# Kernel tuning notes

Measured on AMD Instinct MI355X. Metric: run time of the kernel, lower is better.

The kernel has to match this reference:

```python
import jax, jax.numpy as jnp
import numpy as np

# Forest of B perfect binary trees, depth D levels, M = 2**D - 1 nodes/tree.
B, D, H, X, VOCAB, NCLS = 32, 12, 256, 256, 32000, 20
M = 2 ** D - 1          # 4095 nodes per tree
N = B * M               # 131040 total nodes


def setup_inputs() -> dict:
    key = jax.random.key(0)
    ks = jax.random.split(key, 9)
    x = jax.random.randint(ks[0], (N,), 0, VOCAB, dtype=jnp.int32)
    # leaves are the last level of each tree: in-tree index >= 2**(D-1)-1
    leaf = (jnp.arange(M) >= 2 ** (D - 1) - 1).astype(jnp.int32)
    x_mask = jnp.tile(leaf, B)  # [N] int32, 1 on leaves, 0 on internal nodes
    s = 0.02
    Emb = jax.random.normal(ks[1], (VOCAB, X), jnp.float32) * s
    W_iou = jax.random.normal(ks[2], (3 * H, X), jnp.float32) * s
    b_iou = jnp.zeros((3 * H,), jnp.float32)
    U_iou = jax.random.normal(ks[3], (3 * H, H), jnp.float32) * s
    U_f = jax.random.normal(ks[4], (H, H), jnp.float32) * s
    b_f = jnp.ones((H,), jnp.float32)  # forget-gate bias init
    W_out = jax.random.normal(ks[5], (NCLS, H), jnp.float32) * s
    b_out = jnp.zeros((NCLS,), jnp.float32)
    return {"x": x, "x_mask": x_mask, "Emb": Emb, "W_iou": W_iou,
            "b_iou": b_iou, "U_iou": U_iou, "U_f": U_f, "b_f": b_f,
            "W_out": W_out, "b_out": b_out}


def reference(x, x_mask, Emb, W_iou, b_iou, U_iou, U_f, b_f, W_out, b_out):
    # input_module: embedding applied to masked ids, result masked again
    x_emb = Emb[x * x_mask] * x_mask[:, None].astype(Emb.dtype)      # [N, X]
    xiou = (x_emb @ W_iou.T).reshape(B, M, 3 * H)                    # W_iou * x per node
    h_sum = jnp.zeros((B, M, H), Emb.dtype)    # sum of children h (childsum)
    fc_sum = jnp.zeros((B, M, H), Emb.dtype)   # sum_k f_k * c_k from children
    h_all = jnp.zeros((B, M, H), Emb.dtype)
    # topological propagation: leaves (deepest level) -> roots
    for l in range(D - 1, -1, -1):
        s_, e_ = 2 ** l - 1, 2 ** (l + 1) - 1  # static in-tree level slice
        iou = xiou[:, s_:e_] + h_sum[:, s_:e_] @ U_iou.T + b_iou
        i, o, u = jnp.split(iou, 3, axis=-1)
        c = jax.nn.sigmoid(i) * jnp.tanh(u) + fc_sum[:, s_:e_]
        h = jax.nn.sigmoid(o) * jnp.tanh(c)
        h_all = h_all.at[:, s_:e_].set(h)
        if l > 0:
            f = jax.nn.sigmoid(h @ U_f.T + b_f)          # per-child forget gate
            parents = (np.arange(s_, e_) - 1) // 2       # static parent indices
            h_sum = h_sum.at[:, parents].add(h)
            fc_sum = fc_sum.at[:, parents].add(f * c)
    # output_module applied to all node states
    return h_all.reshape(N, H) @ W_out.T + b_out                    # [N, NCLS]
```

## Files before the change

kernel.cpp:

```cpp
#include <hip/hip_runtime.h>

#define B_TREES 32
#define DEPTH   12
#define M_NODES 4095
#define N_NODES (B_TREES * M_NODES)
#define HDIM    256
#define VOCAB   32000
#define NCLS    20
#define LEAFROWS 65536
#define LDSH_S 20

typedef _Float16 f16;
typedef _Float16 f16x8 __attribute__((ext_vector_type(8)));
typedef _Float16 f16x4 __attribute__((ext_vector_type(4)));
typedef _Float16 f16x2 __attribute__((ext_vector_type(2)));
typedef float    f32x4 __attribute__((ext_vector_type(4)));

__device__ __forceinline__ float sigf(float x)      { return 1.0f / (1.0f + __expf(-x)); }
__device__ __forceinline__ float tanh_fast(float x) { return 1.0f - 2.0f / (1.0f + __expf(2.0f * x)); }

__global__ __launch_bounds__(256) void cvt_kernel(
    const float4* __restrict__ Emb,  const float4* __restrict__ Wiou,
    const float4* __restrict__ Uiou, const float4* __restrict__ Uf,
    const float4* __restrict__ Wout,
    f16x4* __restrict__ Emb16,  f16x4* __restrict__ Wiou16,
    f16x4* __restrict__ Uiou16, f16x4* __restrict__ Uf16,
    f16x4* __restrict__ Wout16)
{
    int i = blockIdx.x * 256 + threadIdx.x;
    if (i < VOCAB * HDIM / 4) {
        float4 v = Emb[i];
        f16x4 r; r[0] = (f16)v.x; r[1] = (f16)v.y; r[2] = (f16)v.z; r[3] = (f16)v.w;
        Emb16[i] = r;
    }
    if (i < 768 * HDIM / 4) {
        float4 v = Wiou[i];
        f16x4 r; r[0] = (f16)v.x; r[1] = (f16)v.y; r[2] = (f16)v.z; r[3] = (f16)v.w;
        Wiou16[i] = r;
        float4 u = Uiou[i];
        f16x4 s; s[0] = (f16)u.x; s[1] = (f16)u.y; s[2] = (f16)u.z; s[3] = (f16)u.w;
        Uiou16[i] = s;
    }
    if (i < HDIM * HDIM / 4) {
        float4 v = Uf[i];
        f16x4 r; r[0] = (f16)v.x; r[1] = (f16)v.y; r[2] = (f16)v.z; r[3] = (f16)v.w;
        Uf16[i] = r;
    }
    if (i < 32 * HDIM / 4) {
        int row = i >> 6;
        f16x4 r = {};
        if (row < NCLS) {
            float4 v = Wout[i];
            r[0] = (f16)v.x; r[1] = (f16)v.y; r[2] = (f16)v.z; r[3] = (f16)v.w;
        }
        Wout16[i] = r;
    }
}

#define VTPW 5
__global__ __launch_bounds__(256) void vocab_kernel(
    const f16* __restrict__ Emb16, const f16* __restrict__ Wiou16,
    const float* __restrict__ b_iou,
    f16* __restrict__ hv, f16* __restrict__ cv)
{
    __shared__ f16 wlds[1536 * 8];
    __shared__ f16 ldshH[4][16 * LDSH_S];
    __shared__ f16 ldshC[4][16 * LDSH_S];

    const int id     = blockIdx.x;
    const int xcd    = id & 7;
    const int slot   = id >> 3;
    const int cg     = slot & 15;
    const int stripe = xcd * 13 + (slot >> 4);
    if (stripe >= 100) return;

    const int tid  = threadIdx.x;
    const int lane = tid & 63;
    const int w    = tid >> 6;
    const int quad = lane >> 4;
    const int l15  = lane & 15;
    const int qk   = quad * 8;
    const int cb0  = cg * 16;

    #pragma unroll
    for (int i = 0; i < 6; ++i) {
        int f = i * 256 + tid;
        int mat = f >> 9, r = f & 511, ks = r >> 6, q = (r >> 4) & 3, c = r & 15;
        *(f16x8*)(wlds + f * 8) = *(const f16x8*)(Wiou16 +
            (mat * 256 + cb0 + c) * HDIM + ks * 32 + q * 8);
    }
    __syncthreads();

    const float bi = b_iou[cb0 + l15];
    const float bo = b_iou[256 + cb0 + l15];
    const float bu = b_iou[512 + cb0 + l15];

    const int row0 = (stripe * 4 + w) * (VTPW * 16);

    f16x8 a[8];
    #pragma unroll
    for (int ks = 0; ks < 8; ++ks)
        a[ks] = *(const f16x8*)(Emb16 + (row0 + l15) * HDIM + ks * 32 + qk);

    for (int rt = 0; rt < VTPW; ++rt) {
        const int rw = row0 + rt * 16;
        f16x8 ac[8];
        #pragma unroll
        for (int ks = 0; ks < 8; ++ks) ac[ks] = a[ks];

        if (rt + 1 < VTPW) {
            #pragma unroll
            for (int ks = 0; ks < 8; ++ks)
                a[ks] = *(const f16x8*)(Emb16 + (rw + 16 + l15) * HDIM + ks * 32 + qk);
        }

        f32x4 acc[3] = {};
        #pragma unroll
        for (int ks = 0; ks < 8; ++ks) {
            #pragma unroll
            for (int mat = 0; mat < 3; ++mat) {
                f16x8 wf = *(const f16x8*)(wlds +
                    ((mat * 8 + ks) * 64 + quad * 16 + l15) * 8);
                acc[mat] = __builtin_amdgcn_mfma_f32_16x16x32_f16(
                    ac[ks], wf, acc[mat], 0, 0, 0);
            }
        }

        #pragma unroll
        for (int r = 0; r < 4; ++r) {
            float i_ = acc[0][r] + bi;
            float o_ = acc[1][r] + bo;
            float u_ = acc[2][r] + bu;
            float c  = sigf(i_) * tanh_fast(u_);
            float h  = sigf(o_) * tanh_fast(c);
            ldshH[w][(quad * 4 + r) * LDSH_S + l15] = (f16)h;
            ldshC[w][(quad * 4 + r) * LDSH_S + l15] = (f16)c;
        }

        {
            int row_l = lane >> 2, cpos = (lane & 3) * 4;
            f16x4 vh = *(const f16x4*)(&ldshH[w][row_l * LDSH_S + cpos]);
            *(f16x4*)(hv + (rw + row_l) * HDIM + cb0 + cpos) = vh;
            f16x4 vc = *(const f16x4*)(&ldshC[w][row_l * LDSH_S + cpos]);
            *(f16x4*)(cv + (rw + row_l) * HDIM + cb0 + cpos) = vc;
        }
    }
}

__global__ __launch_bounds__(256) void vocab_out_kernel(
    const f16* __restrict__ hv, const f16* __restrict__ Wout16,
    const float* __restrict__ bout, float* __restrict__ out_v)
{
    const int lane = threadIdx.x & 63;
    const int w    = threadIdx.x >> 6;
    const int quad = lane >> 4;
    const int l15  = lane & 15;
    const int qk   = quad * 8;

    f16x8 wfk[2][8];
    #pragma unroll
    for (int cf = 0; cf < 2; ++cf)
        #pragma unroll
        for (int ks = 0; ks < 8; ++ks)
            wfk[cf][ks] = *(const f16x8*)(Wout16 +
                (cf * 16 + l15) * HDIM + ks * 32 + qk);
    float bo[2];
    #pragma unroll
    for (int cf = 0; cf < 2; ++cf) {
        int col = cf * 16 + l15;
        bo[cf] = bout[col < NCLS ? col : 0];
    }

    const int tile0 = blockIdx.x * 16;

    for (int rt = w; rt < 16; rt += 4) {
        const int rw = (tile0 + rt) * 16;
        f32x4 acc[2] = {};
        #pragma unroll
        for (int ks = 0; ks < 8; ++ks) {
            f16x8 a = *(const f16x8*)(hv + (rw + l15) * HDIM + ks * 32 + qk);
            #pragma unroll
            for (int cf = 0; cf < 2; ++cf)
                acc[cf] = __builtin_amdgcn_mfma_f32_16x16x32_f16(
                    a, wfk[cf][ks], acc[cf], 0, 0, 0);
        }
        #pragma unroll
        for (int cf = 0; cf < 2; ++cf) {
            const int col = cf * 16 + l15;
            if (col < NCLS) {
                #pragma unroll
                for (int r = 0; r < 4; ++r)
                    out_v[(rw + quad * 4 + r) * NCLS + col] = acc[cf][r] + bo[cf];
            }
        }
    }
}

__global__ __launch_bounds__(256) void leaf_scatter_kernel(
    const int* __restrict__ x, const f16* __restrict__ hv,
    const f16* __restrict__ cv, const float* __restrict__ out_v,
    f16* __restrict__ h16, f16* __restrict__ cT, float* __restrict__ out)
{
    __shared__ int ids[64];
    __shared__ f16 ldsc[64][HDIM + 8];

    const int tid = threadIdx.x;
    const int R0  = blockIdx.x * 64;

    if (tid < 64) {
        int r = R0 + tid;
        int node = (r >> 11) * M_NODES + 2047 + (r & 2047);
        ids[tid] = x[node];
    }
    __syncthreads();

    const int r    = tid >> 2;
    const int p    = tid & 3;
    const int id   = ids[r];
    const int gr   = R0 + r;
    const int node = (gr >> 11) * M_NODES + 2047 + (gr & 2047);

    #pragma unroll
    for (int j = 0; j < 8; ++j) {
        f16x8 v = *(const f16x8*)(hv + id * HDIM + p * 64 + j * 8);
        *(f16x8*)(h16 + node * HDIM + p * 64 + j * 8) = v;
    }
    #pragma unroll
    for (int j = 0; j < 8; ++j) {
        f16x8 v = *(const f16x8*)(cv + id * HDIM + p * 64 + j * 8);
        *(f16x8*)(&ldsc[r][p * 64 + j * 8]) = v;
    }
    #pragma unroll
    for (int j = 0; j < 5; ++j)
        out[node * NCLS + p * 5 + j] = out_v[id * NCLS + p * 5 + j];

    __syncthreads();

    {
        const int c = tid;
        f16 tmp[64];
        #pragma unroll
        for (int rr = 0; rr < 64; ++rr) tmp[rr] = ldsc[rr][c];
        #pragma unroll
        for (int j = 0; j < 8; ++j)
            *(f16x8*)(cT + c * LEAFROWS + R0 + j * 8) = *(const f16x8*)(&tmp[j * 8]);
    }
}

__global__ __launch_bounds__(512)
__attribute__((amdgpu_waves_per_eu(2, 4)))
void fused_level_looped(
    const f16* __restrict__ Uiou16, const f16* __restrict__ Uf16,
    const float* __restrict__ b_iou, const float* __restrict__ b_f,
    f16* __restrict__ h16, const f16* __restrict__ cT_child,
    f16* __restrict__ cT_parent, int l, int rows_p, int nstripes)
{
    __shared__ f16 wlds[2048 * 8];
    __shared__ f16 ldsh[8][16 * LDSH_S];

    const int id   = blockIdx.x;
    const int cg   = (id >> 3) & 15;
    const int spx  = nstripes >> 3;
    const int sbase  = (id & 7) * spx;
    const int sfirst = id >> 7;
    const int scount = spx;

    const int tid  = threadIdx.x;
    const int lane = tid & 63;
    const int w    = tid >> 6;
    const int quad = lane >> 4;
    const int l15  = lane & 15;
    const int qk   = quad * 8;
    const int cb0  = cg * 16;

    #pragma unroll
    for (int i = 0; i < 4; ++i) {
        int f = i * 512 + tid;
        int mat = f >> 9, r = f & 511, ks = r >> 6, q = (r >> 4) & 3, c = r & 15;
        const f16* src = (mat == 0)
            ? (Uf16 + (cb0 + c) * HDIM + ks * 32 + q * 8)
            : (Uiou16 + ((mat - 1) * 256 + cb0 + c) * HDIM + ks * 32 + q * 8);
        *(f16x8*)(wlds + f * 8) = *(const f16x8*)src;
    }
    __syncthreads();

    const float bi  = b_iou[cb0 + l15];
    const float bo  = b_iou[256 + cb0 + l15];
    const float bu  = b_iou[512 + cb0 + l15];
    const float bfv = b_f[cb0 + l15];
    const int lc = l + 1;
    const int maskc = (1 << lc) - 1;
    const int maskp = (1 << l) - 1;
    const int rows_c = rows_p * 2;

    auto cbases = [&](int stripe, int& b0, int& b1) {
        int pw_ = stripe * 128 + w * 16;
        int cw_ = 2 * pw_;
        int cl0 = cw_ + l15;
        b0 = ((cl0 >> lc) * M_NODES + maskc + (cl0 & maskc)) * HDIM;
        int cl1 = cw_ + 16 + l15;
        b1 = ((cl1 >> lc) * M_NODES + maskc + (cl1 & maskc)) * HDIM;
    };

    f16x8 pa0[8], pa1[8];
    {
        int b0, b1;
        cbases(sbase + sfirst, b0, b1);
        #pragma unroll
        for (int ks = 0; ks < 8; ++ks) {
            const int k0 = ks * 32 + qk;
            pa0[ks] = *(const f16x8*)(h16 + b0 + k0);
            pa1[ks] = *(const f16x8*)(h16 + b1 + k0);
        }
    }

    for (int s = sfirst; s < scount; s += 4) {
        const int pw = (sbase + s) * 128 + w * 16;
        const int cw = 2 * pw;
        const bool hasNext = (s + 4 < scount);
        int nb0 = 0, nb1 = 0;
        if (hasNext) cbases(sbase + s + 4, nb0, nb1);

        f16x4 cc0 = *(const f16x4*)(cT_child + (cb0 + l15) * rows_c + cw + quad * 4);
        f16x4 cc1 = *(const f16x4*)(cT_child + (cb0 + l15) * rows_c + cw + 16 + quad * 4);

        f32x4 accf0 = {}, accf1 = {};
        f32x4 au0[3] = {}, au1[3] = {};
        #pragma unroll
        for (int ks = 0; ks < 8; ++ks) {
            const f16x8 a0 = pa0[ks];
            const f16x8 a1 = pa1[ks];
            f16x8 wfF = *(const f16x8*)(wlds + (ks * 64 + quad * 16 + l15) * 8);
            accf0 = __builtin_amdgcn_mfma_f32_16x16x32_f16(a0, wfF, accf0, 0, 0, 0);
            accf1 = __builtin_amdgcn_mfma_f32_16x16x32_f16(a1, wfF, accf1, 0, 0, 0);
            #pragma unroll
            for (int m = 0; m < 3; ++m) {
                f16x8 wm = *(const f16x8*)(wlds +
                    (((m + 1) * 8 + ks) * 64 + quad * 16 + l15) * 8);
                au0[m] = __builtin_amdgcn_mfma_f32_16x16x32_f16(a0, wm, au0[m], 0, 0, 0);
                au1[m] = __builtin_amdgcn_mfma_f32_16x16x32_f16(a1, wm, au1[m], 0, 0, 0);
            }
            if (hasNext) {
                const int k0 = ks * 32 + qk;
                pa0[ks] = *(const f16x8*)(h16 + nb0 + k0);
                pa1[ks] = *(const f16x8*)(h16 + nb1 + k0);
            }
        }

        #pragma unroll
        for (int sh = 0; sh < 2; ++sh) {
            const f32x4& af = sh ? accf1 : accf0;
            const f32x4* au = sh ? au1 : au0;
            f16x4 cc = sh ? cc1 : cc0;
            f16x2 cpack;
            #pragma unroll
            for (int pr = 0; pr < 2; ++pr) {
                float f0 = sigf(af[2 * pr]     + bfv);
                float f1 = sigf(af[2 * pr + 1] + bfv);
                float fc = f0 * (float)cc[2 * pr] + f1 * (float)cc[2 * pr + 1];
                float i_ = au[0][2 * pr] + au[0][2 * pr + 1] + bi;
                float o_ = au[1][2 * pr] + au[1][2 * pr + 1] + bo;
                float u_ = au[2][2 * pr] + au[2][2 * pr + 1] + bu;
                float c  = sigf(i_) * tanh_fast(u_) + fc;
                float h  = sigf(o_) * tanh_fast(c);
                cpack[pr] = (f16)c;
                ldsh[w][(sh * 8 + quad * 2 + pr) * LDSH_S + l15] = (f16)h;
            }
            *(f16x2*)(cT_parent + (cb0 + l15) * rows_p + pw + sh * 8 + quad * 2) = cpack;
        }

        {
            int prow = lane >> 2, cpos = (lane & 3) * 4;
            int p = pw + prow;
            int b = p >> l, tt = p & maskp;
            int node = b * M_NODES + (1 << l) - 1 + tt;
            f16x4 v = *(const f16x4*)(&ldsh[w][prow * LDSH_S + cpos]);
            *(f16x4*)(h16 + node * HDIM + cb0 + cpos) = v;
        }
    }
}

__global__ __launch_bounds__(512) void fused_level_small(
    const f16* __restrict__ Uiou16, const f16* __restrict__ Uf16,
    const float* __restrict__ b_iou, const float* __restrict__ b_f,
    f16* __restrict__ h16, const f16* __restrict__ cT_child,
    f16* __restrict__ cT_parent, int l, int rows_p)
{
    __shared__ f16 wlds[2048 * 8];
    __shared__ f16 ldsh[8][16 * LDSH_S];

    const int id = blockIdx.x;
    const int cg    = id & 15;
    const int sbase = id >> 4;

    const int tid  = threadIdx.x;
    const int lane = tid & 63;
    const int w    = tid >> 6;
    const int quad = lane >> 4;
    const int l15  = lane & 15;
    const int qk   = quad * 8;
    const int cb0  = cg * 16;

    #pragma unroll
    for (int i = 0; i < 4; ++i) {
        int f = i * 512 + tid;
        int mat = f >> 9, r = f & 511, ks = r >> 6, q = (r >> 4) & 3, c = r & 15;
        const f16* src = (mat == 0)
            ? (Uf16 + (cb0 + c) * HDIM + ks * 32 + q * 8)
            : (Uiou16 + ((mat - 1) * 256 + cb0 + c) * HDIM + ks * 32 + q * 8);
        *(f16x8*)(wlds + f * 8) = *(const f16x8*)src;
    }
    __syncthreads();

    const float bi  = b_iou[cb0 + l15];
    const float bo  = b_iou[256 + cb0 + l15];
    const float bu  = b_iou[512 + cb0 + l15];
    const float bfv = b_f[cb0 + l15];
    const int lc = l + 1;
    const int maskc = (1 << lc) - 1;
    const int maskp = (1 << l) - 1;
    const int rows_c = rows_p * 2;

    const int pw = sbase * 128 + w * 16;
    if (pw >= rows_p) return;
    const int cw = 2 * pw;

    int childBase0, childBase1;
    {
        int cl0 = cw + l15;
        childBase0 = ((cl0 >> lc) * M_NODES + maskc + (cl0 & maskc)) * HDIM;
        int cl1 = cw + 16 + l15;
        childBase1 = ((cl1 >> lc) * M_NODES + maskc + (cl1 & maskc)) * HDIM;
    }

    f32x4 accf0 = {}, accf1 = {};
    f32x4 au0[3] = {}, au1[3] = {};
    #pragma unroll
    for (int ks = 0; ks < 8; ++ks) {
        const int k0 = ks * 32 + qk;
        f16x8 a0 = *(const f16x8*)(h16 + childBase0 + k0);
        f16x8 a1 = *(const f16x8*)(h16 + childBase1 + k0);
        f16x8 wfF = *(const f16x8*)(wlds + (ks * 64 + quad * 16 + l15) * 8);
        accf0 = __builtin_amdgcn_mfma_f32_16x16x32_f16(a0, wfF, accf0, 0, 0, 0);
        accf1 = __builtin_amdgcn_mfma_f32_16x16x32_f16(a1, wfF, accf1, 0, 0, 0);
        #pragma unroll
        for (int m = 0; m < 3; ++m) {
            f16x8 wm = *(const f16x8*)(wlds +
                (((m + 1) * 8 + ks) * 64 + quad * 16 + l15) * 8);
            au0[m] = __builtin_amdgcn_mfma_f32_16x16x32_f16(a0, wm, au0[m], 0, 0, 0);
            au1[m] = __builtin_amdgcn_mfma_f32_16x16x32_f16(a1, wm, au1[m], 0, 0, 0);
        }
    }

    #pragma unroll
    for (int sh = 0; sh < 2; ++sh) {
        const f32x4& af = sh ? accf1 : accf0;
        const f32x4* au = sh ? au1 : au0;
        const int csr = cw + sh * 16;
        f16x4 cc = *(const f16x4*)(cT_child +
            (cb0 + l15) * rows_c + csr + quad * 4);
        f16x2 cpack;
        #pragma unroll
        for (int pr = 0; pr < 2; ++pr) {
            float f0 = sigf(af[2 * pr]     + bfv);
            float f1 = sigf(af[2 * pr + 1] + bfv);
            float fc = f0 * (float)cc[2 * pr] + f1 * (float)cc[2 * pr + 1];
            float i_ = au[0][2 * pr] + au[0][2 * pr + 1] + bi;
            float o_ = au[1][2 * pr] + au[1][2 * pr + 1] + bo;
            float u_ = au[2][2 * pr] + au[2][2 * pr + 1] + bu;
            float c  = sigf(i_) * tanh_fast(u_) + fc;
            float h  = sigf(o_) * tanh_fast(c);
            cpack[pr] = (f16)c;
            ldsh[w][(sh * 8 + quad * 2 + pr) * LDSH_S + l15] = (f16)h;
        }
        *(f16x2*)(cT_parent + (cb0 + l15) * rows_p + pw + sh * 8 + quad * 2) = cpack;
    }

    {
        int prow = lane >> 2, cpos = (lane & 3) * 4;
        int p = pw + prow;
        int b = p >> l, tt = p & maskp;
        int node = b * M_NODES + (1 << l) - 1 + tt;
        f16x4 v = *(const f16x4*)(&ldsh[w][prow * LDSH_S + cpos]);
        *(f16x4*)(h16 + node * HDIM + cb0 + cpos) = v;
    }
}

__global__ __launch_bounds__(256) void out_kernel(
    const f16* __restrict__ h16, const f16* __restrict__ Wout16,
    const float* __restrict__ bout, float* __restrict__ out)
{
    const int lane = threadIdx.x & 63;
    const int w    = threadIdx.x >> 6;
    const int quad = lane >> 4;
    const int l15  = lane & 15;
    const int qk   = quad * 8;

    f16x8 wfk[2][8];
    #pragma unroll
    for (int cf = 0; cf < 2; ++cf)
        #pragma unroll
        for (int ks = 0; ks < 8; ++ks)
            wfk[cf][ks] = *(const f16x8*)(Wout16 +
                (cf * 16 + l15) * HDIM + ks * 32 + qk);
    float bo[2];
    #pragma unroll
    for (int cf = 0; cf < 2; ++cf) {
        int col = cf * 16 + l15;
        bo[cf] = bout[col < NCLS ? col : 0];
    }

    const int tile0 = blockIdx.x * 16;

    for (int rt = w; rt < 16; rt += 4) {
        const int tt = tile0 + rt;
        const int rw = (tt >> 7) * M_NODES + (tt & 127) * 16;
        f32x4 acc[2] = {};
        #pragma unroll
        for (int ks = 0; ks < 8; ++ks) {
            f16x8 a = *(const f16x8*)(h16 + (rw + l15) * HDIM + ks * 32 + qk);
            #pragma unroll
            for (int cf = 0; cf < 2; ++cf)
                acc[cf] = __builtin_amdgcn_mfma_f32_16x16x32_f16(
                    a, wfk[cf][ks], acc[cf], 0, 0, 0);
        }
        #pragma unroll
        for (int cf = 0; cf < 2; ++cf) {
            const int col = cf * 16 + l15;
            if (col < NCLS) {
                #pragma unroll
                for (int r = 0; r < 4; ++r)
                    out[(rw + quad * 4 + r) * NCLS + col] = acc[cf][r] + bo[cf];
            }
        }
    }
}

extern "C" void kernel_launch(void* const* d_in, const int* in_sizes, int n_in,
                              void* d_out, int out_size, void* d_ws, size_t ws_size,
                              hipStream_t stream)
{
    const int*   x     = (const int*)d_in[0];
    const float* Emb   = (const float*)d_in[2];
    const float* W_iou = (const float*)d_in[3];
    const float* b_iou = (const float*)d_in[4];
    const float* U_iou = (const float*)d_in[5];
    const float* U_f   = (const float*)d_in[6];
    const float* b_f   = (const float*)d_in[7];
    const float* W_out = (const float*)d_in[8];
    const float* b_out = (const float*)d_in[9];
    float* out = (float*)d_out;

    char* ws = (char*)d_ws;
    size_t off = 0;
    auto take = [&](size_t bytes) -> char* {
        char* p = ws + off; off += (bytes + 255) & ~(size_t)255; return p;
    };
    f16* h16    = (f16*)take((size_t)N_NODES * HDIM * 2);
    f16* cA     = (f16*)take((size_t)HDIM * LEAFROWS * 2);
    f16* cB     = (f16*)take((size_t)HDIM * (LEAFROWS / 2) * 2);
    f16* Emb16  = (f16*)take((size_t)VOCAB * HDIM * 2);
    f16* Wiou16 = (f16*)take((size_t)768 * HDIM * 2);
    f16* Uiou16 = (f16*)take((size_t)768 * HDIM * 2);
    f16* Uf16   = (f16*)take((size_t)HDIM * HDIM * 2);
    f16* Wout16 = (f16*)take((size_t)32 * HDIM * 2);
    f16* cv     = (f16*)take((size_t)VOCAB * HDIM * 2);
    float* outv = (float*)take((size_t)VOCAB * NCLS * 4);
    f16* hv     = cB;

    cvt_kernel<<<VOCAB * HDIM / 4 / 256, 256, 0, stream>>>(
        (const float4*)Emb, (const float4*)W_iou, (const float4*)U_iou,
        (const float4*)U_f, (const float4*)W_out,
        (f16x4*)Emb16, (f16x4*)Wiou16, (f16x4*)Uiou16, (f16x4*)Uf16,
        (f16x4*)Wout16);

    vocab_kernel<<<8 * 13 * 16, 256, 0, stream>>>(
        Emb16, Wiou16, b_iou, hv, cv);

    vocab_out_kernel<<<dim3(VOCAB / 16 / 16), 256, 0, stream>>>(
        hv, Wout16, b_out, outv);

    leaf_scatter_kernel<<<dim3(LEAFROWS / 64), 256, 0, stream>>>(
        x, hv, cv, outv, h16, cA, out);

    f16* cin  = cA;
    f16* cout_ = cB;
    for (int l = 10; l >= 0; --l) {
        int rows_p = B_TREES << l;
        int nstripes = (rows_p + 127) / 128;
        if (l >= 8) {
            fused_level_looped<<<512, 512, 0, stream>>>(
                Uiou16, Uf16, b_iou, b_f, h16, cin, cout_, l, rows_p, nstripes);
        } else {
            fused_level_small<<<nstripes * 16, 512, 0, stream>>>(
                Uiou16, Uf16, b_iou, b_f, h16, cin, cout_, l, rows_p);
        }
        f16* t = cin; cin = cout_; cout_ = t;
    }

    out_kernel<<<dim3(32 * 128 / 16), 256, 0, stream>>>(
        h16, Wout16, b_out, out);
}
```

Before: 420.6 us.

## Fuse top five tree levels into one per-tree kernel, drop prefetch pipeline

Levels 4..0 are now processed by a single kernel with one block per tree, using __syncthreads between levels instead of five separate kernel launches. Each tree's parent data lives in its own block, so no cross-block sync is needed. The per-level weights are read straight from global memory rather than staged in LDS. The looped level kernel also loses its register prefetch of the next stripe's child rows and its waves_per_eu attribute, which may cost latency hiding. Only 32 blocks run the tail, so parallelism there is low, but launch overhead for the tiny levels goes away.

Measured after the change: 483.4 us. +14.9%, slower.

```diff
diff --git a/kernel.cpp b/kernel.cpp
--- a/kernel.cpp
+++ b/kernel.cpp
@@ -247,9 +247,7 @@
     }
 }
 
-__global__ __launch_bounds__(512)
-__attribute__((amdgpu_waves_per_eu(2, 4)))
-void fused_level_looped(
+__global__ __launch_bounds__(512) void fused_level_looped(
     const f16* __restrict__ Uiou16, const f16* __restrict__ Uf16,
     const float* __restrict__ b_iou, const float* __restrict__ b_f,
     f16* __restrict__ h16, const f16* __restrict__ cT_child,
@@ -293,43 +291,26 @@
     const int maskp = (1 << l) - 1;
     const int rows_c = rows_p * 2;
 
-    auto cbases = [&](int stripe, int& b0, int& b1) {
-        int pw_ = stripe * 128 + w * 16;
-        int cw_ = 2 * pw_;
-        int cl0 = cw_ + l15;
-        b0 = ((cl0 >> lc) * M_NODES + maskc + (cl0 & maskc)) * HDIM;
-        int cl1 = cw_ + 16 + l15;
-        b1 = ((cl1 >> lc) * M_NODES + maskc + (cl1 & maskc)) * HDIM;
-    };
-
-    f16x8 pa0[8], pa1[8];
-    {
-        int b0, b1;
-        cbases(sbase + sfirst, b0, b1);
+    for (int s = sfirst; s < scount; s += 4) {
+        const int stripe = sbase + s;
+        const int pw = stripe * 128 + w * 16;
+        const int cw = 2 * pw;
+
+        int childBase0, childBase1;
+        {
+            int cl0 = cw + l15;
+            childBase0 = ((cl0 >> lc) * M_NODES + maskc + (cl0 & maskc)) * HDIM;
+            int cl1 = cw + 16 + l15;
+            childBase1 = ((cl1 >> lc) * M_NODES + maskc + (cl1 & maskc)) * HDIM;
+        }
+
+        f32x4 accf0 = {}, accf1 = {};
+        f32x4 au0[3] = {}, au1[3] = {};
         #pragma unroll
         for (int ks = 0; ks < 8; ++ks) {
             const int k0 = ks * 32 + qk;
-            pa0[ks] = *(const f16x8*)(h16 + b0 + k0);
-            pa1[ks] = *(const f16x8*)(h16 + b1 + k0);
-        }
-    }
-
-    for (int s = sfirst; s < scount; s += 4) {
-        const int pw = (sbase + s) * 128 + w * 16;
-        const int cw = 2 * pw;
-        const bool hasNext = (s + 4 < scount);
-        int nb0 = 0, nb1 = 0;
-        if (hasNext) cbases(sbase + s + 4, nb0, nb1);
-
-        f16x4 cc0 = *(const f16x4*)(cT_child + (cb0 + l15) * rows_c + cw + quad * 4);
-        f16x4 cc1 = *(const f16x4*)(cT_child + (cb0 + l15) * rows_c + cw + 16 + quad * 4);
-
-        f32x4 accf0 = {}, accf1 = {};
-        f32x4 au0[3] = {}, au1[3] = {};
-        #pragma unroll
-        for (int ks = 0; ks < 8; ++ks) {
-            const f16x8 a0 = pa0[ks];
-            const f16x8 a1 = pa1[ks];
+            f16x8 a0 = *(const f16x8*)(h16 + childBase0 + k0);
+            f16x8 a1 = *(const f16x8*)(h16 + childBase1 + k0);
             f16x8 wfF = *(const f16x8*)(wlds + (ks * 64 + quad * 16 + l15) * 8);
             accf0 = __builtin_amdgcn_mfma_f32_16x16x32_f16(a0, wfF, accf0, 0, 0, 0);
             accf1 = __builtin_amdgcn_mfma_f32_16x16x32_f16(a1, wfF, accf1, 0, 0, 0);
@@ -340,18 +321,15 @@
                 au0[m] = __builtin_amdgcn_mfma_f32_16x16x32_f16(a0, wm, au0[m], 0, 0, 0);
                 au1[m] = __builtin_amdgcn_mfma_f32_16x16x32_f16(a1, wm, au1[m], 0, 0, 0);
             }
-            if (hasNext) {
-                const int k0 = ks * 32 + qk;
-                pa0[ks] = *(const f16x8*)(h16 + nb0 + k0);
-                pa1[ks] = *(const f16x8*)(h16 + nb1 + k0);
-            }
         }
 
         #pragma unroll
         for (int sh = 0; sh < 2; ++sh) {
             const f32x4& af = sh ? accf1 : accf0;
             const f32x4* au = sh ? au1 : au0;
-            f16x4 cc = sh ? cc1 : cc0;
+            const int csr = cw + sh * 16;
+            f16x4 cc = *(const f16x4*)(cT_child +
+                (cb0 + l15) * rows_c + csr + quad * 4);
             f16x2 cpack;
             #pragma unroll
             for (int pr = 0; pr < 2; ++pr) {
@@ -483,6 +461,110 @@
         int node = b * M_NODES + (1 << l) - 1 + tt;
         f16x4 v = *(const f16x4*)(&ldsh[w][prow * LDSH_S + cpos]);
         *(f16x4*)(h16 + node * HDIM + cb0 + cpos) = v;
+    }
+}
+
+__global__ __launch_bounds__(512) void fused_tail_kernel(
+    const f16* __restrict__ Uiou16, const f16* __restrict__ Uf16,
+    const float* __restrict__ b_iou, const float* __restrict__ b_f,
+    f16* __restrict__ h16, const f16* __restrict__ cT_in,
+    f16* __restrict__ ctail)
+{
+    __shared__ f16 ldsh[8][16 * LDSH_S];
+
+    const int b    = blockIdx.x;
+    const int tid  = threadIdx.x;
+    const int lane = tid & 63;
+    const int w    = tid >> 6;
+    const int quad = lane >> 4;
+    const int l15  = lane & 15;
+    const int qk   = quad * 8;
+
+    const int coff[5] = {245760, 229376, 196608, 131072, 0};
+
+    for (int l = 4; l >= 0; --l) {
+        const int rows_t  = 1 << l;
+        const int crows_t = rows_t * 2;
+        const int rows_p  = B_TREES << l;
+        const int rows_c  = rows_p * 2;
+        const int lc = l + 1;
+        const int maskc = (1 << lc) - 1;
+        const int maskp = (1 << l) - 1;
+
+        const f16* cread = (l == 4) ? cT_in : (ctail + coff[l + 1]);
+        f16*       cwrit = ctail + coff[l];
+
+        #pragma unroll
+        for (int pass = 0; pass < 2; ++pass) {
+            const int cg  = w + pass * 8;
+            const int cb0 = cg * 16;
+
+            const float bi  = b_iou[cb0 + l15];
+            const float bo  = b_iou[256 + cb0 + l15];
+            const float bu  = b_iou[512 + cb0 + l15];
+            const float bfv = b_f[cb0 + l15];
+
+            int cl0l = l15;      if (cl0l >= crows_t) cl0l = crows_t - 1;
+            int cl1l = 16 + l15; if (cl1l >= crows_t) cl1l = crows_t - 1;
+            const int cg0 = b * crows_t + cl0l;
+            const int cg1 = b * crows_t + cl1l;
+            const int childBase0 = ((cg0 >> lc) * M_NODES + maskc + (cg0 & maskc)) * HDIM;
+            const int childBase1 = ((cg1 >> lc) * M_NODES + maskc + (cg1 & maskc)) * HDIM;
+
+            f32x4 accf0 = {}, accf1 = {};
+            f32x4 au0[3] = {}, au1[3] = {};
+            #pragma unroll
+            for (int ks = 0; ks < 8; ++ks) {
+                const int k0 = ks * 32 + qk;
+                f16x8 a0 = *(const f16x8*)(h16 + childBase0 + k0);
+                f16x8 a1 = *(const f16x8*)(h16 + childBase1 + k0);
+                f16x8 wfF = *(const f16x8*)(Uf16 + (cb0 + l15) * HDIM + k0);
+                accf0 = __builtin_amdgcn_mfma_f32_16x16x32_f16(a0, wfF, accf0, 0, 0, 0);
+                accf1 = __builtin_amdgcn_mfma_f32_16x16x32_f16(a1, wfF, accf1, 0, 0, 0);
+                #pragma unroll
+                for (int m = 0; m < 3; ++m) {
+                    f16x8 wm = *(const f16x8*)(Uiou16 + (m * 256 + cb0 + l15) * HDIM + k0);
+                    au0[m] = __builtin_amdgcn_mfma_f32_16x16x32_f16(a0, wm, au0[m], 0, 0, 0);
+                    au1[m] = __builtin_amdgcn_mfma_f32_16x16x32_f16(a1, wm, au1[m], 0, 0, 0);
+                }
+            }
+
+            #pragma unroll
+            for (int sh = 0; sh < 2; ++sh) {
+                const f32x4& af = sh ? accf1 : accf0;
+                const f32x4* au = sh ? au1 : au0;
+                #pragma unroll
+                for (int pr = 0; pr < 2; ++pr) {
+                    const int j = sh * 8 + quad * 2 + pr;
+                    if (j < rows_t) {
+                        f16 c0 = cread[(cb0 + l15) * rows_c + b * crows_t + 2 * j];
+                        f16 c1 = cread[(cb0 + l15) * rows_c + b * crows_t + 2 * j + 1];
+                        float f0 = sigf(af[2 * pr]     + bfv);
+                        float f1 = sigf(af[2 * pr + 1] + bfv);
+                        float fc = f0 * (float)c0 + f1 * (float)c1;
+                        float i_ = au[0][2 * pr] + au[0][2 * pr + 1] + bi;
+                        float o_ = au[1][2 * pr] + au[1][2 * pr + 1] + bo;
+                        float u_ = au[2][2 * pr] + au[2][2 * pr + 1] + bu;
+                        float c  = sigf(i_) * tanh_fast(u_) + fc;
+                        float h  = sigf(o_) * tanh_fast(c);
+                        cwrit[(cb0 + l15) * rows_p + b * rows_t + j] = (f16)c;
+                        ldsh[w][j * LDSH_S + l15] = (f16)h;
+                    }
+                }
+            }
+
+            {
+                int prow = lane >> 2, cpos = (lane & 3) * 4;
+                if (prow < rows_t) {
+                    int gp = b * rows_t + prow;
+                    int node = (gp >> l) * M_NODES + (1 << l) - 1 + (gp & maskp);
+                    f16x4 v = *(const f16x4*)(&ldsh[w][prow * LDSH_S + cpos]);
+                    *(f16x4*)(h16 + node * HDIM + cb0 + cpos) = v;
+                }
+            }
+        }
+
+        __syncthreads();
     }
 }
 
@@ -566,6 +648,7 @@
     f16* Wout16 = (f16*)take((size_t)32 * HDIM * 2);
     f16* cv     = (f16*)take((size_t)VOCAB * HDIM * 2);
     float* outv = (float*)take((size_t)VOCAB * NCLS * 4);
+    f16* ctail  = (f16*)take((size_t)256 * 1024 * 2);
     f16* hv     = cB;
 
     cvt_kernel<<<VOCAB * HDIM / 4 / 256, 256, 0, stream>>>(
@@ -585,7 +668,7 @@
 
     f16* cin  = cA;
     f16* cout_ = cB;
-    for (int l = 10; l >= 0; --l) {
+    for (int l = 10; l >= 5; --l) {
         int rows_p = B_TREES << l;
         int nstripes = (rows_p + 127) / 128;
         if (l >= 8) {
@@ -598,6 +681,9 @@
         f16* t = cin; cin = cout_; cout_ = t;
     }
 
+    fused_tail_kernel<<<32, 512, 0, stream>>>(
+        Uiou16, Uf16, b_iou, b_f, h16, cin, ctail);
+
     out_kernel<<<dim3(32 * 128 / 16), 256, 0, stream>>>(
         h16, Wout16, b_out, out);
 }
```
